# Optimization experiments

Measured on AMD Instinct MI355X. Metric: run time of the kernel, lower is better.

## Reference

```python
import jax, jax.numpy as jnp
import numpy as np

V, E, HD, NT = 50001, 256, 512, 24   # vocab, embed_dim, hidden_dim, tag_size
H = HD // 2                          # per-direction LSTM hidden
B, S = 64, 512


def setup_inputs() -> dict:
    key = jax.random.key(0)
    ks = jax.random.split(key, 18)
    lw = lambda k, sh, s=0.05: (jax.random.normal(k, sh, jnp.float32) * s)
    x = jax.random.randint(ks[0], (B, S), 0, V).astype(jnp.int32)
    lengths = jax.random.randint(ks[1], (B,), S // 2, S + 1)
    mask = jnp.arange(S)[None, :] < lengths[:, None]  # [B,S] bool, mask[:,0]=True
    return {
        "x": x,
        "mask": mask,
        "emb": lw(ks[2], (V, E), 0.1),
        "Wih_f": lw(ks[3], (4 * H, E)), "Whh_f": lw(ks[4], (4 * H, H)),
        "bih_f": lw(ks[5], (4 * H,)), "bhh_f": lw(ks[6], (4 * H,)),
        "Wih_b": lw(ks[7], (4 * H, E)), "Whh_b": lw(ks[8], (4 * H, H)),
        "bih_b": lw(ks[9], (4 * H,)), "bhh_b": lw(ks[10], (4 * H,)),
        "Wout": lw(ks[11], (NT, HD)), "bout": lw(ks[12], (NT,)),
        "trans": lw(ks[13], (NT, NT), 0.1),
        "start": lw(ks[14], (NT,), 0.1),
        "end": lw(ks[15], (NT,), 0.1),
    }


def _lstm_dir(xs, Wih, Whh, bih, bhh):
    # xs: [S, B, E] -> hs: [S, B, H]; torch gate order i, f, g, o
    Bn = xs.shape[1]
    h0 = jnp.zeros((Bn, H), xs.dtype)

    def step(carry, xt):
        h, c = carry
        g = xt @ Wih.T + h @ Whh.T + bih + bhh
        i, f, gg, o = jnp.split(g, 4, axis=-1)
        c = jax.nn.sigmoid(f) * c + jax.nn.sigmoid(i) * jnp.tanh(gg)
        h = jax.nn.sigmoid(o) * jnp.tanh(c)
        return (h, c), h

    _, hs = jax.lax.scan(step, (h0, h0), xs)
    return hs


def _viterbi(emissions, mask, trans, start, end):
    # emissions: [B, S, T]; mask: [B, S] bool. Returns (tags [B,S] int, best_score [B]).
    em = emissions.transpose(1, 0, 2)   # [S, B, T]
    mk = mask.transpose(1, 0)           # [S, B]
    nT = trans.shape[0]
    idx_id = jnp.arange(nT)[None, :]    # identity backpointers for padded steps
    score = start[None, :] + em[0]      # [B, T]

    def step(score, inp):
        e_t, m_t = inp
        cand = score[:, :, None] + trans[None, :, :] + e_t[:, None, :]  # [B,Tprev,Tnext]
        idx = jnp.argmax(cand, axis=1)
        best = jnp.max(cand, axis=1)
        idx = jnp.where(m_t[:, None], idx, idx_id)
        new_score = jnp.where(m_t[:, None], best, score)
        return new_score, idx

    score, hist = jax.lax.scan(step, score, (em[1:], mk[1:]))  # hist: [S-1, B, T]
    final = score + end[None, :]
    last_tag = jnp.argmax(final, axis=1)   # [B]
    best_score = jnp.max(final, axis=1)    # [B]

    def back(tag, h_t):
        prev = jnp.take_along_axis(h_t, tag[:, None], axis=1)[:, 0]
        return prev, tag

    tag0, ys = jax.lax.scan(back, last_tag, hist, reverse=True)
    tags = jnp.concatenate([tag0[None, :], ys], axis=0).T  # [B, S]
    return tags, best_score


def reference(x, mask, emb, Wih_f, Whh_f, bih_f, bhh_f, Wih_b, Whh_b, bih_b, bhh_b,
              Wout, bout, trans, start, end):
    e = emb[x]                      # [B, S, E] embedding gather
    xs = e.transpose(1, 0, 2)       # [S, B, E] time-major for scan
    hf = _lstm_dir(xs, Wih_f, Whh_f, bih_f, bhh_f)
    hb = jnp.flip(_lstm_dir(jnp.flip(xs, 0), Wih_b, Whh_b, bih_b, bhh_b), 0)
    h = jnp.concatenate([hf, hb], axis=-1)          # [S, B, HD]
    emis = (h @ Wout.T + bout).transpose(1, 0, 2)   # [B, S, T]
    tags, _ = _viterbi(emis, mask, trans, start, end)
    return tags
```

## Files before the change

### kernel.cpp

```cpp
#include <hip/hip_runtime.h>
#include <math.h>

#define B_   64
#define S_   512
#define E_   256
#define H_   256
#define G4H_ 1024
#define NT_  24

static const size_t HBUF_OFF  = 0;
static const size_t CST_OFF   = 131072;
static const size_t EMF_OFF   = 163840;
static const size_t EMB_OFF   = 950272;
static const size_t HOUT_OFF  = 1736704;

__device__ __forceinline__ float sigmoidf_(float x) {
  return 1.0f / (1.0f + expf(-x));
}

__global__ __launch_bounds__(256) void k1_xpre(
    const int* __restrict__ x, const float* __restrict__ emb,
    const float* __restrict__ Wih_f, const float* __restrict__ bih_f,
    const float* __restrict__ bhh_f, const float* __restrict__ Wih_b,
    const float* __restrict__ bih_b, const float* __restrict__ bhh_b,
    float* __restrict__ xpre_c, int chunk, int tc)
{
  __shared__ float As[32][132];
  __shared__ float Bs[32][132];
  __shared__ int   xt[128];

  const int tid = threadIdx.x;
  const int wg  = blockIdx.x;
  const int per_dir = 4 * tc;
  const int d   = wg / per_dir;
  const int rem = wg % per_dir;
  const int m0  = (rem >> 3) * 128;
  const int n0  = (rem & 7) * 128;
  const int t0  = chunk * tc;

  const float* Wih = d ? Wih_b : Wih_f;
  const float* bih = d ? bih_b : bih_f;
  const float* bhh = d ? bhh_b : bhh_f;

  if (tid < 128) {
    int m = m0 + tid;
    int lt = m >> 6, b = m & 63;
    int tok = d ? (S_ - 1 - (t0 + lt)) : (t0 + lt);
    xt[tid] = x[b * S_ + tok];
  }
  __syncthreads();

  float acc[8][8];
#pragma unroll
  for (int i = 0; i < 8; ++i)
#pragma unroll
    for (int j = 0; j < 8; ++j) acc[i][j] = 0.0f;

  const int mt8 = tid & 15;
  const int nt8 = tid >> 4;
  const int q = tid & 7, rbase = tid >> 3;

  for (int kc = 0; kc < 8; ++kc) {
    const int k0 = kc * 32;
#pragma unroll
    for (int i = 0; i < 4; ++i) {
      int row = rbase + i * 32;
      float4 a = *(const float4*)(emb + (long)xt[row] * E_ + k0 + q * 4);
      As[q * 4 + 0][row] = a.x; As[q * 4 + 1][row] = a.y;
      As[q * 4 + 2][row] = a.z; As[q * 4 + 3][row] = a.w;
      float4 w = *(const float4*)(Wih + (long)(n0 + row) * E_ + k0 + q * 4);
      Bs[q * 4 + 0][row] = w.x; Bs[q * 4 + 1][row] = w.y;
      Bs[q * 4 + 2][row] = w.z; Bs[q * 4 + 3][row] = w.w;
    }
    __syncthreads();
#pragma unroll
    for (int k = 0; k < 32; ++k) {
      float4 a0 = *(float4*)&As[k][mt8 * 8];
      float4 a1 = *(float4*)&As[k][mt8 * 8 + 4];
      float4 b0 = *(float4*)&Bs[k][nt8 * 8];
      float4 b1 = *(float4*)&Bs[k][nt8 * 8 + 4];
      float am[8] = {a0.x, a0.y, a0.z, a0.w, a1.x, a1.y, a1.z, a1.w};
      float bn[8] = {b0.x, b0.y, b0.z, b0.w, b1.x, b1.y, b1.z, b1.w};
#pragma unroll
      for (int i = 0; i < 8; ++i)
#pragma unroll
        for (int j = 0; j < 8; ++j) acc[i][j] = fmaf(am[i], bn[j], acc[i][j]);
    }
    __syncthreads();
  }

  float bias[8];
  {
    float4 u0 = *(const float4*)(bih + n0 + nt8 * 8);
    float4 u1 = *(const float4*)(bih + n0 + nt8 * 8 + 4);
    float4 v0 = *(const float4*)(bhh + n0 + nt8 * 8);
    float4 v1 = *(const float4*)(bhh + n0 + nt8 * 8 + 4);
    bias[0] = u0.x + v0.x; bias[1] = u0.y + v0.y; bias[2] = u0.z + v0.z;
    bias[3] = u0.w + v0.w; bias[4] = u1.x + v1.x; bias[5] = u1.y + v1.y;
    bias[6] = u1.z + v1.z; bias[7] = u1.w + v1.w;
  }
#pragma unroll
  for (int i = 0; i < 8; ++i) {
    int m = m0 + mt8 * 8 + i;
    int lt = m >> 6, b = m & 63;
    float* o = xpre_c + ((size_t)(d * tc + lt) * B_ + b) * G4H_ + n0 + nt8 * 8;
    float4 r0, r1;
    r0.x = acc[i][0] + bias[0]; r0.y = acc[i][1] + bias[1];
    r0.z = acc[i][2] + bias[2]; r0.w = acc[i][3] + bias[3];
    r1.x = acc[i][4] + bias[4]; r1.y = acc[i][5] + bias[5];
    r1.z = acc[i][6] + bias[6]; r1.w = acc[i][7] + bias[7];
    *(float4*)o = r0;
    *(float4*)(o + 4) = r1;
  }
}

__global__ __launch_bounds__(256, 1) void k2_lstm(
    const float* __restrict__ Whh_f, const float* __restrict__ Whh_b,
    const float* __restrict__ xpre_c, float* __restrict__ hout_c,
    unsigned long long* hbuf, float* cstate, int chunk, int tc)
{
  __shared__ float hTb[16][260];
  __shared__ float part[2][4][16][36];

  const int tid = threadIdx.x;
  const int wg  = blockIdx.x;
  const int d   = wg >> 7;
  const int bg  = (wg >> 5) & 3;
  const int s   = wg & 31;
  const int b0  = bg * 16;
  const float* Whh = d ? Whh_b : Whh_f;

  const int w     = tid >> 6;
  const int lane  = tid & 63;
  const int bl16  = lane & 15;
  const int kb    = lane >> 4;
  const int kbase = w * 64 + kb * 16;
  const int ks    = tid >> 5;
  const int tl    = tid & 31, bt = tl & 3, rt = tl >> 2;
  const int pbl   = tid >> 3, pj = tid & 7;

  float wreg[4][32];
#pragma unroll
  for (int ri = 0; ri < 4; ++ri) {
    int r = rt * 4 + ri, g = r >> 3, j = r & 7;
    const float* src = Whh + ((size_t)(g * H_ + s * 8 + j)) * H_ + ks * 32;
#pragma unroll
    for (int q = 0; q < 8; ++q) {
      float4 v = *(const float4*)(src + q * 4);
      wreg[ri][q * 4 + 0] = v.x; wreg[ri][q * 4 + 1] = v.y;
      wreg[ri][q * 4 + 2] = v.z; wreg[ri][q * 4 + 3] = v.w;
    }
  }

  float c_reg = 0.0f;
  if (chunk > 0 && tid < 128)
    c_reg = cstate[((size_t)d * B_ + b0 + pbl) * H_ + s * 8 + pj];

  for (int tt = 1; tt <= tc; ++tt) {
    const int t  = chunk * tc + tt;
    const int lt = tt - 1;
    const int p  = tt & 1;

    float xp[4];
    if (tid < 128) {
#pragma unroll
      for (int g = 0; g < 4; ++g)
        xp[g] = xpre_c[((size_t)(d * tc + lt) * B_ + b0 + pbl) * G4H_ +
                       g * H_ + s * 8 + pj];
    }

    {
      const unsigned expt = (unsigned)(t - 1);
      const unsigned long long* hb =
          hbuf + ((size_t)(((t - 1) & 1) * 2 + d)) * (256 * 64);
      const size_t a0 = (size_t)kbase * 64 + b0 + bl16;
      unsigned long long e[16];
#pragma unroll
      for (int i = 0; i < 16; ++i)
        e[i] = __hip_atomic_load(hb + a0 + (size_t)i * 64,
                                 __ATOMIC_RELAXED, __HIP_MEMORY_SCOPE_AGENT);
      int lim = 0;
      while (true) {
        unsigned bad = 0;
#pragma unroll
        for (int i = 0; i < 16; ++i)
          if ((unsigned)(e[i] >> 32) != expt) bad |= (1u << i);
        if (bad == 0) break;
        if (++lim > (1 << 18)) break;
#pragma unroll
        for (int i = 0; i < 16; ++i)
          if (bad & (1u << i))
            e[i] = __hip_atomic_load(hb + a0 + (size_t)i * 64,
                                     __ATOMIC_RELAXED,
                                     __HIP_MEMORY_SCOPE_AGENT);
      }
      float4 v0, v1, v2, v3;
      v0.x = __uint_as_float((unsigned)e[0]);  v0.y = __uint_as_float((unsigned)e[1]);
      v0.z = __uint_as_float((unsigned)e[2]);  v0.w = __uint_as_float((unsigned)e[3]);
      v1.x = __uint_as_float((unsigned)e[4]);  v1.y = __uint_as_float((unsigned)e[5]);
      v1.z = __uint_as_float((unsigned)e[6]);  v1.w = __uint_as_float((unsigned)e[7]);
      v2.x = __uint_as_float((unsigned)e[8]);  v2.y = __uint_as_float((unsigned)e[9]);
      v2.z = __uint_as_float((unsigned)e[10]); v2.w = __uint_as_float((unsigned)e[11]);
      v3.x = __uint_as_float((unsigned)e[12]); v3.y = __uint_as_float((unsigned)e[13]);
      v3.z = __uint_as_float((unsigned)e[14]); v3.w = __uint_as_float((unsigned)e[15]);
      *(float4*)&hTb[bl16][kbase +  0] = v0;
      *(float4*)&hTb[bl16][kbase +  4] = v1;
      *(float4*)&hTb[bl16][kbase +  8] = v2;
      *(float4*)&hTb[bl16][kbase + 12] = v3;
    }

    float acc[4][4];
#pragma unroll
    for (int bi = 0; bi < 4; ++bi)
#pragma unroll
      for (int ri = 0; ri < 4; ++ri) acc[bi][ri] = 0.0f;
#pragma unroll
    for (int kq = 0; kq < 8; ++kq) {
      const int k0 = ks * 32 + kq * 4;
      float4 h4[4];
#pragma unroll
      for (int bi = 0; bi < 4; ++bi)
        h4[bi] = *(float4*)&hTb[bt * 4 + bi][k0];
#pragma unroll
      for (int kk = 0; kk < 4; ++kk) {
#pragma unroll
        for (int bi = 0; bi < 4; ++bi) {
          const float hv = kk == 0 ? h4[bi].x : kk == 1 ? h4[bi].y
                         : kk == 2 ? h4[bi].z : h4[bi].w;
#pragma unroll
          for (int ri = 0; ri < 4; ++ri)
            acc[bi][ri] = fmaf(hv, wreg[ri][kq * 4 + kk], acc[bi][ri]);
        }
      }
    }
#pragma unroll
    for (int bi = 0; bi < 4; ++bi)
#pragma unroll
      for (int ri = 0; ri < 4; ++ri)
        acc[bi][ri] += __shfl_xor(acc[bi][ri], 32, 64);
    if (lane < 32) {
#pragma unroll
      for (int bi = 0; bi < 4; ++bi) {
        float4 v = make_float4(acc[bi][0], acc[bi][1], acc[bi][2], acc[bi][3]);
        *(float4*)&part[p][w][bt * 4 + bi][rt * 4] = v;
      }
    }
    __syncthreads();

    if (tid < 128) {
      const int bglob = b0 + pbl;
      float gsum[4];
#pragma unroll
      for (int g = 0; g < 4; ++g) {
        const int r = g * 8 + pj;
        gsum[g] = xp[g] + ((part[p][0][pbl][r] + part[p][1][pbl][r]) +
                           (part[p][2][pbl][r] + part[p][3][pbl][r]));
      }
      float si = sigmoidf_(gsum[0]);
      float sf = sigmoidf_(gsum[1]);
      float tg = tanhf(gsum[2]);
      float so = sigmoidf_(gsum[3]);
      c_reg = sf * c_reg + si * tg;
      float h = so * tanhf(c_reg);
      unsigned long long pk =
          (((unsigned long long)(unsigned)t) << 32) |
          (unsigned long long)__float_as_uint(h);
      __hip_atomic_store(hbuf + ((size_t)((t & 1) * 2 + d)) * (256 * 64) +
                             (size_t)(s * 8 + pj) * 64 + bglob,
                         pk, __ATOMIC_RELAXED, __HIP_MEMORY_SCOPE_AGENT);
      hout_c[((size_t)(d * tc + lt) * B_ + bglob) * H_ + s * 8 + pj] = h;
    }
  }

  if (tid < 128)
    cstate[((size_t)d * B_ + b0 + pbl) * H_ + s * 8 + pj] = c_reg;
}

__global__ __launch_bounds__(256) void k3_emis(
    const float* __restrict__ hout_c, const float* __restrict__ Wout,
    float* __restrict__ emisF, float* __restrict__ emisB, int chunk, int tc)
{
  __shared__ float hh[8][264];
  const int tid = threadIdx.x;
  const int nt8 = tc >> 3;
  const int per_d = 64 * nt8;
  const int d   = blockIdx.x / per_d;
  const int rem = blockIdx.x % per_d;
  const int b   = rem / nt8;
  const int lt0 = (rem % nt8) * 8;
  float* emisX = d ? emisB : emisF;
  {
    int r = tid >> 5, q = tid & 31;
    const float* src = hout_c + ((size_t)(d * tc + lt0 + r) * B_ + b) * H_;
#pragma unroll
    for (int i = 0; i < 2; ++i) {
      int f4i = q + 32 * i;
      *(float4*)&hh[r][f4i * 4] = *(const float4*)(src + f4i * 4);
    }
  }
  __syncthreads();
  if (tid < 192) {
    int r = tid / 24, tag = tid % 24;
    float acc = 0.0f;
    const float* w = Wout + (size_t)tag * 512 + d * 256;
#pragma unroll 4
    for (int k4 = 0; k4 < 64; ++k4) {
      float4 wv = *(const float4*)(w + k4 * 4);
      float4 hv = *(const float4*)&hh[r][k4 * 4];
      acc = fmaf(wv.x, hv.x, acc);
      acc = fmaf(wv.y, hv.y, acc);
      acc = fmaf(wv.z, hv.z, acc);
      acc = fmaf(wv.w, hv.w, acc);
    }
    int lt = lt0 + r;
    int tok = d ? (S_ - 1 - (chunk * tc + lt)) : (chunk * tc + lt);
    emisX[((size_t)b * S_ + tok) * NT_ + tag] = acc;
  }
}

__global__ __launch_bounds__(64) void k4_viterbi(
    const float* __restrict__ emisF, const float* __restrict__ emisB,
    const float* __restrict__ bout, const unsigned char* __restrict__ mb,
    const float* __restrict__ trans, const float* __restrict__ startv,
    const float* __restrict__ endv, int* __restrict__ outp)
{
  __shared__ float tl[24 * 25];
  __shared__ float sc[24];
  __shared__ float fin[24];
  __shared__ unsigned char hist[511 * 24];
  const int b = blockIdx.x;
  const int tid = threadIdx.x;
  const int is_bool = mb[1];

  for (int i = tid; i < 576; i += 64) tl[(i / 24) * 25 + (i % 24)] = trans[i];
  if (tid < 24) {
    size_t e0 = (size_t)b * S_ * NT_ + tid;
    sc[tid] = startv[tid] + (emisF[e0] + emisB[e0] + bout[tid]);
  }
  __syncthreads();

  for (int t = 1; t < S_; ++t) {
    float best = -3.4e38f, scj = 0.f;
    int idx = 0;
    int m;
    {
      int mi = b * S_ + t;
      m = is_bool ? (int)mb[mi] : (int)mb[mi << 2];
    }
    if (tid < 24) {
      size_t ei = ((size_t)b * S_ + t) * NT_ + tid;
      float e = emisF[ei] + emisB[ei] + bout[tid];
      for (int i = 0; i < 24; ++i) {
        float v = (sc[i] + tl[i * 25 + tid]) + e;
        if (v > best) { best = v; idx = i; }
      }
      scj = sc[tid];
    }
    __syncthreads();
    if (tid < 24) {
      sc[tid] = m ? best : scj;
      hist[(t - 1) * 24 + tid] = (unsigned char)(m ? idx : tid);
    }
    __syncthreads();
  }
  if (tid < 24) fin[tid] = sc[tid] + endv[tid];
  __syncthreads();
  if (tid == 0) {
    int tag = 0; float best = fin[0];
    for (int i = 1; i < 24; ++i)
      if (fin[i] > best) { best = fin[i]; tag = i; }
    outp[b * S_ + (S_ - 1)] = tag;
    for (int tt = S_ - 2; tt >= 0; --tt) {
      tag = hist[tt * 24 + tag];
      outp[b * S_ + tt] = tag;
    }
  }
}

extern "C" void kernel_launch(void* const* d_in, const int* in_sizes, int n_in,
                              void* d_out, int out_size, void* d_ws,
                              size_t ws_size, hipStream_t stream)
{
  const int*   x      = (const int*)d_in[0];
  const unsigned char* maskb = (const unsigned char*)d_in[1];
  const float* emb    = (const float*)d_in[2];
  const float* Wih_f  = (const float*)d_in[3];
  const float* Whh_f  = (const float*)d_in[4];
  const float* bih_f  = (const float*)d_in[5];
  const float* bhh_f  = (const float*)d_in[6];
  const float* Wih_b  = (const float*)d_in[7];
  const float* Whh_b  = (const float*)d_in[8];
  const float* bih_b  = (const float*)d_in[9];
  const float* bhh_b  = (const float*)d_in[10];
  const float* Wout   = (const float*)d_in[11];
  const float* bout   = (const float*)d_in[12];
  const float* trans  = (const float*)d_in[13];
  const float* startv = (const float*)d_in[14];
  const float* endv   = (const float*)d_in[15];

  int tc = 8;
  {
    const int cand[6] = {512, 256, 128, 64, 32, 16};
    for (int i = 0; i < 6; ++i) {
      size_t needF = HOUT_OFF + (size_t)cand[i] * (2 * B_ * H_ + 2 * B_ * G4H_);
      if (needF * sizeof(float) <= ws_size) { tc = cand[i]; break; }
    }
  }
  const int nc = S_ / tc;

  float* ws     = (float*)d_ws;
  unsigned long long* hbuf = (unsigned long long*)(ws + HBUF_OFF);
  float* cstate = ws + CST_OFF;
  float* emisF  = ws + EMF_OFF;
  float* emisB  = ws + EMB_OFF;
  float* hout_c = ws + HOUT_OFF;
  float* xpre_c = hout_c + (size_t)tc * 2 * B_ * H_;

  hipMemsetAsync(d_ws, 0, 131072 * sizeof(float), stream);

  for (int c = 0; c < nc; ++c) {
    hipLaunchKernelGGL(k1_xpre, dim3(8 * tc), dim3(256), 0, stream,
                       x, emb, Wih_f, bih_f, bhh_f, Wih_b, bih_b, bhh_b,
                       xpre_c, c, tc);
    hipLaunchKernelGGL(k2_lstm, dim3(256), dim3(256), 0, stream,
                       Whh_f, Whh_b, xpre_c, hout_c, hbuf, cstate, c, tc);
    hipLaunchKernelGGL(k3_emis, dim3(2 * 64 * (tc / 8)), dim3(256), 0, stream,
                       hout_c, Wout, emisF, emisB, c, tc);
  }
  hipLaunchKernelGGL(k4_viterbi, dim3(64), dim3(64), 0, stream,
                     emisF, emisB, bout, maskb, trans, startv, endv,
                     (int*)d_out);
}
```

Baseline: 2.885 ms.

## Give each wave its own batch slice in LSTM step to drop block barrier

Restructures the recurrent LSTM kernel so each of the four waves owns 4 batch rows and the full K=256 reduction, instead of splitting K across waves. Partial sums are reduced with intra-wave shuffles, and the per-step __syncthreads plus the cross-wave shared-memory reduction are removed. A rotated k order in the weight load and h reads is added to reduce LDS bank conflicts. The trade-off is three shuffle rounds per accumulator in place of one, and reliance on wave-synchronous LDS visibility between the gbuf write and read within a wave.

```diff
diff --git a/kernel.cpp b/kernel.cpp
--- a/kernel.cpp
+++ b/kernel.cpp
@@ -119,53 +119,50 @@
     const float* __restrict__ xpre_c, float* __restrict__ hout_c,
     unsigned long long* hbuf, float* cstate, int chunk, int tc)
 {
-  __shared__ float hTb[16][260];
-  __shared__ float part[2][4][16][36];
-
-  const int tid = threadIdx.x;
-  const int wg  = blockIdx.x;
-  const int d   = wg >> 7;
-  const int bg  = (wg >> 5) & 3;
-  const int s   = wg & 31;
-  const int b0  = bg * 16;
+  __shared__ float hTb[4][4][264];
+  __shared__ float gbuf[4][4][36];
+
+  const int tid  = threadIdx.x;
+  const int wg   = blockIdx.x;
+  const int d    = wg >> 7;
+  const int bg   = (wg >> 5) & 3;
+  const int s    = wg & 31;
   const float* Whh = d ? Whh_b : Whh_f;
 
-  const int w     = tid >> 6;
-  const int lane  = tid & 63;
-  const int bl16  = lane & 15;
-  const int kb    = lane >> 4;
-  const int kbase = w * 64 + kb * 16;
-  const int ks    = tid >> 5;
-  const int tl    = tid & 31, bt = tl & 3, rt = tl >> 2;
-  const int pbl   = tid >> 3, pj = tid & 7;
+  const int w    = tid >> 6;
+  const int lane = tid & 63;
+  const int bw   = bg * 16 + 4 * w;
+  const int kg = lane >> 3, rp = lane & 7;
+  const int sb = lane & 3, ksec = lane >> 2;
+  const int pb = (lane >> 3) & 3, pj = lane & 7;
 
   float wreg[4][32];
 #pragma unroll
   for (int ri = 0; ri < 4; ++ri) {
-    int r = rt * 4 + ri, g = r >> 3, j = r & 7;
-    const float* src = Whh + ((size_t)(g * H_ + s * 8 + j)) * H_ + ks * 32;
+    int r = rp * 4 + ri, g = r >> 3, j = r & 7;
+    const float* src = Whh + ((size_t)(g * H_ + s * 8 + j)) * H_ + kg * 32;
 #pragma unroll
     for (int q = 0; q < 8; ++q) {
-      float4 v = *(const float4*)(src + q * 4);
+      int qs = (q + kg * 2) & 7;
+      float4 v = *(const float4*)(src + qs * 4);
       wreg[ri][q * 4 + 0] = v.x; wreg[ri][q * 4 + 1] = v.y;
       wreg[ri][q * 4 + 2] = v.z; wreg[ri][q * 4 + 3] = v.w;
     }
   }
 
   float c_reg = 0.0f;
-  if (chunk > 0 && tid < 128)
-    c_reg = cstate[((size_t)d * B_ + b0 + pbl) * H_ + s * 8 + pj];
+  if (chunk > 0 && lane < 32)
+    c_reg = cstate[((size_t)d * B_ + bw + pb) * H_ + s * 8 + pj];
 
   for (int tt = 1; tt <= tc; ++tt) {
     const int t  = chunk * tc + tt;
     const int lt = tt - 1;
-    const int p  = tt & 1;
 
     float xp[4];
-    if (tid < 128) {
+    if (lane < 32) {
 #pragma unroll
       for (int g = 0; g < 4; ++g)
-        xp[g] = xpre_c[((size_t)(d * tc + lt) * B_ + b0 + pbl) * G4H_ +
+        xp[g] = xpre_c[((size_t)(d * tc + lt) * B_ + bw + pb) * G4H_ +
                        g * H_ + s * 8 + pj];
     }
 
@@ -173,7 +170,7 @@
       const unsigned expt = (unsigned)(t - 1);
       const unsigned long long* hb =
           hbuf + ((size_t)(((t - 1) & 1) * 2 + d)) * (256 * 64);
-      const size_t a0 = (size_t)kbase * 64 + b0 + bl16;
+      const size_t a0 = (size_t)(ksec * 16) * 64 + (bw + sb);
       unsigned long long e[16];
 #pragma unroll
       for (int i = 0; i < 16; ++i)
@@ -194,68 +191,62 @@
                                      __ATOMIC_RELAXED,
                                      __HIP_MEMORY_SCOPE_AGENT);
       }
-      float4 v0, v1, v2, v3;
-      v0.x = __uint_as_float((unsigned)e[0]);  v0.y = __uint_as_float((unsigned)e[1]);
-      v0.z = __uint_as_float((unsigned)e[2]);  v0.w = __uint_as_float((unsigned)e[3]);
-      v1.x = __uint_as_float((unsigned)e[4]);  v1.y = __uint_as_float((unsigned)e[5]);
-      v1.z = __uint_as_float((unsigned)e[6]);  v1.w = __uint_as_float((unsigned)e[7]);
-      v2.x = __uint_as_float((unsigned)e[8]);  v2.y = __uint_as_float((unsigned)e[9]);
-      v2.z = __uint_as_float((unsigned)e[10]); v2.w = __uint_as_float((unsigned)e[11]);
-      v3.x = __uint_as_float((unsigned)e[12]); v3.y = __uint_as_float((unsigned)e[13]);
-      v3.z = __uint_as_float((unsigned)e[14]); v3.w = __uint_as_float((unsigned)e[15]);
-      *(float4*)&hTb[bl16][kbase +  0] = v0;
-      *(float4*)&hTb[bl16][kbase +  4] = v1;
-      *(float4*)&hTb[bl16][kbase +  8] = v2;
-      *(float4*)&hTb[bl16][kbase + 12] = v3;
+#pragma unroll
+      for (int n = 0; n < 4; ++n) {
+        float4 v;
+        v.x = __uint_as_float((unsigned)e[4 * n + 0]);
+        v.y = __uint_as_float((unsigned)e[4 * n + 1]);
+        v.z = __uint_as_float((unsigned)e[4 * n + 2]);
+        v.w = __uint_as_float((unsigned)e[4 * n + 3]);
+        *(float4*)&hTb[w][sb][ksec * 16 + n * 4] = v;
+      }
     }
 
     float acc[4][4];
 #pragma unroll
-    for (int bi = 0; bi < 4; ++bi)
-#pragma unroll
-      for (int ri = 0; ri < 4; ++ri) acc[bi][ri] = 0.0f;
-#pragma unroll
-    for (int kq = 0; kq < 8; ++kq) {
-      const int k0 = ks * 32 + kq * 4;
-      float4 h4[4];
-#pragma unroll
-      for (int bi = 0; bi < 4; ++bi)
-        h4[bi] = *(float4*)&hTb[bt * 4 + bi][k0];
-#pragma unroll
-      for (int kk = 0; kk < 4; ++kk) {
-#pragma unroll
-        for (int bi = 0; bi < 4; ++bi) {
-          const float hv = kk == 0 ? h4[bi].x : kk == 1 ? h4[bi].y
-                         : kk == 2 ? h4[bi].z : h4[bi].w;
+    for (int b = 0; b < 4; ++b)
+#pragma unroll
+      for (int ri = 0; ri < 4; ++ri) acc[b][ri] = 0.0f;
+#pragma unroll
+    for (int b = 0; b < 4; ++b) {
+      const float* hrow = &hTb[w][b][kg * 32];
+#pragma unroll
+      for (int q = 0; q < 8; ++q) {
+        int qs = (q + kg * 2) & 7;
+        float4 h4 = *(const float4*)(hrow + qs * 4);
+#pragma unroll
+        for (int kk = 0; kk < 4; ++kk) {
+          const float hv = kk == 0 ? h4.x : kk == 1 ? h4.y
+                         : kk == 2 ? h4.z : h4.w;
 #pragma unroll
           for (int ri = 0; ri < 4; ++ri)
-            acc[bi][ri] = fmaf(hv, wreg[ri][kq * 4 + kk], acc[bi][ri]);
+            acc[b][ri] = fmaf(hv, wreg[ri][q * 4 + kk], acc[b][ri]);
         }
       }
     }
 #pragma unroll
-    for (int bi = 0; bi < 4; ++bi)
-#pragma unroll
-      for (int ri = 0; ri < 4; ++ri)
-        acc[bi][ri] += __shfl_xor(acc[bi][ri], 32, 64);
+    for (int b = 0; b < 4; ++b)
+#pragma unroll
+      for (int ri = 0; ri < 4; ++ri) {
+        float v = acc[b][ri];
+        v += __shfl_xor(v, 8, 64);
+        v += __shfl_xor(v, 16, 64);
+        v += __shfl_xor(v, 32, 64);
+        acc[b][ri] = v;
+      }
+    if (kg == 0) {
+#pragma unroll
+      for (int b = 0; b < 4; ++b)
+        *(float4*)&gbuf[w][b][rp * 4] =
+            make_float4(acc[b][0], acc[b][1], acc[b][2], acc[b][3]);
+    }
+
     if (lane < 32) {
-#pragma unroll
-      for (int bi = 0; bi < 4; ++bi) {
-        float4 v = make_float4(acc[bi][0], acc[bi][1], acc[bi][2], acc[bi][3]);
-        *(float4*)&part[p][w][bt * 4 + bi][rt * 4] = v;
-      }
-    }
-    __syncthreads();
-
-    if (tid < 128) {
-      const int bglob = b0 + pbl;
+      const int bglob = bw + pb;
       float gsum[4];
 #pragma unroll
-      for (int g = 0; g < 4; ++g) {
-        const int r = g * 8 + pj;
-        gsum[g] = xp[g] + ((part[p][0][pbl][r] + part[p][1][pbl][r]) +
-                           (part[p][2][pbl][r] + part[p][3][pbl][r]));
-      }
+      for (int g = 0; g < 4; ++g)
+        gsum[g] = xp[g] + gbuf[w][pb][g * 8 + pj];
       float si = sigmoidf_(gsum[0]);
       float sf = sigmoidf_(gsum[1]);
       float tg = tanhf(gsum[2]);
@@ -272,8 +263,8 @@
     }
   }
 
-  if (tid < 128)
-    cstate[((size_t)d * B_ + b0 + pbl) * H_ + s * 8 + pj] = c_reg;
+  if (lane < 32)
+    cstate[((size_t)d * B_ + bw + pb) * H_ + s * 8 + pj] = c_reg;
 }
 
 __global__ __launch_bounds__(256) void k3_emis(
```

New measurement: 4.461 ms. 1.55x slower.

## Use split-bf16 MFMA for input projection GEMM

Applied to the files above, without the earlier changes.

Replaces the FP32 FMA tiled GEMM that computes the input-gate preactivations with a bf16 MFMA version. Both operands are split into hi and lo bf16 parts, and three or four MFMAs per tile recover near-FP32 accuracy. A new pre-kernel converts Wih into the hi/lo bf16 arrays once per call. Workspace offsets shift to make room for these arrays. The sequential LSTM kernel likely dominates runtime, so the overall effect is limited. The output stores are scalar and strided rather than vectorized.

```diff
diff --git a/kernel.cpp b/kernel.cpp
--- a/kernel.cpp
+++ b/kernel.cpp
@@ -10,24 +10,58 @@
 
 static const size_t HBUF_OFF  = 0;
 static const size_t CST_OFF   = 131072;
-static const size_t EMF_OFF   = 163840;
-static const size_t EMB_OFF   = 950272;
-static const size_t HOUT_OFF  = 1736704;
+static const size_t WHI_OFF   = 163840;
+static const size_t WLO_OFF   = 425984;
+static const size_t EMF_OFF   = 688128;
+static const size_t EMB_OFF   = 1474560;
+static const size_t HOUT_OFF  = 2260992;
+
+typedef short  bf16x8_ __attribute__((ext_vector_type(8)));
+typedef float  f32x4_  __attribute__((ext_vector_type(4)));
 
 __device__ __forceinline__ float sigmoidf_(float x) {
   return 1.0f / (1.0f + expf(-x));
 }
 
-__global__ __launch_bounds__(256) void k1_xpre(
+__device__ __forceinline__ unsigned short bf16_rne_(float v) {
+  unsigned u = __float_as_uint(v);
+  unsigned r = u + 0x7fffu + ((u >> 16) & 1u);
+  return (unsigned short)(r >> 16);
+}
+
+__global__ __launch_bounds__(256) void k0_wconv(
+    const float* __restrict__ Wf, const float* __restrict__ Wb,
+    unsigned short* __restrict__ whi, unsigned short* __restrict__ wlo)
+{
+  int idx = blockIdx.x * 256 + threadIdx.x;
+  int d   = idx >> 16;
+  int i4  = idx & 65535;
+  const float* W = d ? Wb : Wf;
+  float4 v = *(const float4*)(W + (size_t)i4 * 4);
+  float vv[4] = {v.x, v.y, v.z, v.w};
+  unsigned short h[4], l[4];
+#pragma unroll
+  for (int e = 0; e < 4; ++e) {
+    h[e] = bf16_rne_(vv[e]);
+    float hf = __uint_as_float((unsigned)h[e] << 16);
+    l[e] = bf16_rne_(vv[e] - hf);
+  }
+  size_t o = (size_t)d * 262144 + (size_t)i4 * 4;
+  whi[o + 0] = h[0]; whi[o + 1] = h[1]; whi[o + 2] = h[2]; whi[o + 3] = h[3];
+  wlo[o + 0] = l[0]; wlo[o + 1] = l[1]; wlo[o + 2] = l[2]; wlo[o + 3] = l[3];
+}
+
+__global__ __launch_bounds__(256) void k1_xpre_mfma(
     const int* __restrict__ x, const float* __restrict__ emb,
-    const float* __restrict__ Wih_f, const float* __restrict__ bih_f,
-    const float* __restrict__ bhh_f, const float* __restrict__ Wih_b,
+    const unsigned short* __restrict__ whi,
+    const unsigned short* __restrict__ wlo,
+    const float* __restrict__ bih_f, const float* __restrict__ bhh_f,
     const float* __restrict__ bih_b, const float* __restrict__ bhh_b,
     float* __restrict__ xpre_c, int chunk, int tc)
 {
-  __shared__ float As[32][132];
-  __shared__ float Bs[32][132];
-  __shared__ int   xt[128];
+  __shared__ unsigned short Ahi[128][40], Alo[128][40];
+  __shared__ unsigned short Bhi[128][40], Blo[128][40];
+  __shared__ int xt[128];
 
   const int tid = threadIdx.x;
   const int wg  = blockIdx.x;
@@ -38,9 +72,10 @@
   const int n0  = (rem & 7) * 128;
   const int t0  = chunk * tc;
 
-  const float* Wih = d ? Wih_b : Wih_f;
   const float* bih = d ? bih_b : bih_f;
   const float* bhh = d ? bhh_b : bhh_f;
+  const unsigned short* Whi = whi + (size_t)d * 262144;
+  const unsigned short* Wlo = wlo + (size_t)d * 262144;
 
   if (tid < 128) {
     int m = m0 + tid;
@@ -48,70 +83,95 @@
     int tok = d ? (S_ - 1 - (t0 + lt)) : (t0 + lt);
     xt[tid] = x[b * S_ + tok];
   }
-  __syncthreads();
-
-  float acc[8][8];
-#pragma unroll
-  for (int i = 0; i < 8; ++i)
-#pragma unroll
-    for (int j = 0; j < 8; ++j) acc[i][j] = 0.0f;
-
-  const int mt8 = tid & 15;
-  const int nt8 = tid >> 4;
-  const int q = tid & 7, rbase = tid >> 3;
-
-  for (int kc = 0; kc < 8; ++kc) {
-    const int k0 = kc * 32;
-#pragma unroll
-    for (int i = 0; i < 4; ++i) {
-      int row = rbase + i * 32;
-      float4 a = *(const float4*)(emb + (long)xt[row] * E_ + k0 + q * 4);
-      As[q * 4 + 0][row] = a.x; As[q * 4 + 1][row] = a.y;
-      As[q * 4 + 2][row] = a.z; As[q * 4 + 3][row] = a.w;
-      float4 w = *(const float4*)(Wih + (long)(n0 + row) * E_ + k0 + q * 4);
-      Bs[q * 4 + 0][row] = w.x; Bs[q * 4 + 1][row] = w.y;
-      Bs[q * 4 + 2][row] = w.z; Bs[q * 4 + 3][row] = w.w;
-    }
+
+  const int lane = tid & 63, wid = tid >> 6;
+  const int wr = wid >> 1, wc = wid & 1;
+  const int fr = lane & 15, fq = lane >> 4;
+  const int sr = tid >> 1, sh = tid & 1;
+
+  f32x4_ acc[4][4];
+#pragma unroll
+  for (int i = 0; i < 4; ++i)
+#pragma unroll
+    for (int j = 0; j < 4; ++j) acc[i][j] = (f32x4_){0.f, 0.f, 0.f, 0.f};
+
+  for (int slab = 0; slab < 8; ++slab) {
+    const int k0 = slab * 32;
     __syncthreads();
-#pragma unroll
-    for (int k = 0; k < 32; ++k) {
-      float4 a0 = *(float4*)&As[k][mt8 * 8];
-      float4 a1 = *(float4*)&As[k][mt8 * 8 + 4];
-      float4 b0 = *(float4*)&Bs[k][nt8 * 8];
-      float4 b1 = *(float4*)&Bs[k][nt8 * 8 + 4];
-      float am[8] = {a0.x, a0.y, a0.z, a0.w, a1.x, a1.y, a1.z, a1.w};
-      float bn[8] = {b0.x, b0.y, b0.z, b0.w, b1.x, b1.y, b1.z, b1.w};
-#pragma unroll
-      for (int i = 0; i < 8; ++i)
-#pragma unroll
-        for (int j = 0; j < 8; ++j) acc[i][j] = fmaf(am[i], bn[j], acc[i][j]);
+    {
+      const float* src = emb + (size_t)xt[sr] * E_ + k0 + sh * 16;
+      unsigned short h[16], l[16];
+#pragma unroll
+      for (int q = 0; q < 4; ++q) {
+        float4 v = *(const float4*)(src + q * 4);
+        float vv[4] = {v.x, v.y, v.z, v.w};
+#pragma unroll
+        for (int e = 0; e < 4; ++e) {
+          h[q * 4 + e] = bf16_rne_(vv[e]);
+          float hf = __uint_as_float((unsigned)h[q * 4 + e] << 16);
+          l[q * 4 + e] = bf16_rne_(vv[e] - hf);
+        }
+      }
+      *(bf16x8_*)&Ahi[sr][sh * 16 + 0] = *(bf16x8_*)&h[0];
+      *(bf16x8_*)&Ahi[sr][sh * 16 + 8] = *(bf16x8_*)&h[8];
+      *(bf16x8_*)&Alo[sr][sh * 16 + 0] = *(bf16x8_*)&l[0];
+      *(bf16x8_*)&Alo[sr][sh * 16 + 8] = *(bf16x8_*)&l[8];
+    }
+    {
+      const size_t o = (size_t)(n0 + sr) * E_ + k0 + sh * 16;
+      *(bf16x8_*)&Bhi[sr][sh * 16 + 0] = *(const bf16x8_*)(Whi + o);
+      *(bf16x8_*)&Bhi[sr][sh * 16 + 8] = *(const bf16x8_*)(Whi + o + 8);
+      *(bf16x8_*)&Blo[sr][sh * 16 + 0] = *(const bf16x8_*)(Wlo + o);
+      *(bf16x8_*)&Blo[sr][sh * 16 + 8] = *(const bf16x8_*)(Wlo + o + 8);
     }
     __syncthreads();
-  }
-
-  float bias[8];
-  {
-    float4 u0 = *(const float4*)(bih + n0 + nt8 * 8);
-    float4 u1 = *(const float4*)(bih + n0 + nt8 * 8 + 4);
-    float4 v0 = *(const float4*)(bhh + n0 + nt8 * 8);
-    float4 v1 = *(const float4*)(bhh + n0 + nt8 * 8 + 4);
-    bias[0] = u0.x + v0.x; bias[1] = u0.y + v0.y; bias[2] = u0.z + v0.z;
-    bias[3] = u0.w + v0.w; bias[4] = u1.x + v1.x; bias[5] = u1.y + v1.y;
-    bias[6] = u1.z + v1.z; bias[7] = u1.w + v1.w;
-  }
-#pragma unroll
-  for (int i = 0; i < 8; ++i) {
-    int m = m0 + mt8 * 8 + i;
-    int lt = m >> 6, b = m & 63;
-    float* o = xpre_c + ((size_t)(d * tc + lt) * B_ + b) * G4H_ + n0 + nt8 * 8;
-    float4 r0, r1;
-    r0.x = acc[i][0] + bias[0]; r0.y = acc[i][1] + bias[1];
-    r0.z = acc[i][2] + bias[2]; r0.w = acc[i][3] + bias[3];
-    r1.x = acc[i][4] + bias[4]; r1.y = acc[i][5] + bias[5];
-    r1.z = acc[i][6] + bias[6]; r1.w = acc[i][7] + bias[7];
-    *(float4*)o = r0;
-    *(float4*)(o + 4) = r1;
-  }
+
+    bf16x8_ ah[4], al[4], bh[4], bl[4];
+#pragma unroll
+    for (int mi = 0; mi < 4; ++mi) {
+      int row = 64 * wr + mi * 16 + fr;
+      ah[mi] = *(bf16x8_*)&Ahi[row][fq * 8];
+      al[mi] = *(bf16x8_*)&Alo[row][fq * 8];
+    }
+#pragma unroll
+    for (int ni = 0; ni < 4; ++ni) {
+      int row = 64 * wc + ni * 16 + fr;
+      bh[ni] = *(bf16x8_*)&Bhi[row][fq * 8];
+      bl[ni] = *(bf16x8_*)&Blo[row][fq * 8];
+    }
+#pragma unroll
+    for (int mi = 0; mi < 4; ++mi)
+#pragma unroll
+      for (int ni = 0; ni < 4; ++ni) {
+        acc[mi][ni] = __builtin_amdgcn_mfma_f32_16x16x32_bf16(
+            al[mi], bl[ni], acc[mi][ni], 0, 0, 0);
+        acc[mi][ni] = __builtin_amdgcn_mfma_f32_16x16x32_bf16(
+            al[mi], bh[ni], acc[mi][ni], 0, 0, 0);
+        acc[mi][ni] = __builtin_amdgcn_mfma_f32_16x16x32_bf16(
+            ah[mi], bl[ni], acc[mi][ni], 0, 0, 0);
+        acc[mi][ni] = __builtin_amdgcn_mfma_f32_16x16x32_bf16(
+            ah[mi], bh[ni], acc[mi][ni], 0, 0, 0);
+      }
+  }
+
+  float bias[4];
+#pragma unroll
+  for (int ni = 0; ni < 4; ++ni) {
+    int col = n0 + 64 * wc + ni * 16 + fr;
+    bias[ni] = bih[col] + bhh[col];
+  }
+  const size_t base = (size_t)(d * tc * 64) * G4H_;
+#pragma unroll
+  for (int mi = 0; mi < 4; ++mi)
+#pragma unroll
+    for (int ni = 0; ni < 4; ++ni) {
+      int col = n0 + 64 * wc + ni * 16 + fr;
+#pragma unroll
+      for (int r = 0; r < 4; ++r) {
+        int m = m0 + 64 * wr + mi * 16 + fq * 4 + r;
+        xpre_c[base + (size_t)m * G4H_ + col] = acc[mi][ni][r] + bias[ni];
+      }
+    }
 }
 
 __global__ __launch_bounds__(256, 1) void k2_lstm(
@@ -411,16 +471,20 @@
   float* ws     = (float*)d_ws;
   unsigned long long* hbuf = (unsigned long long*)(ws + HBUF_OFF);
   float* cstate = ws + CST_OFF;
+  unsigned short* whi = (unsigned short*)(ws + WHI_OFF);
+  unsigned short* wlo = (unsigned short*)(ws + WLO_OFF);
   float* emisF  = ws + EMF_OFF;
   float* emisB  = ws + EMB_OFF;
   float* hout_c = ws + HOUT_OFF;
   float* xpre_c = hout_c + (size_t)tc * 2 * B_ * H_;
 
   hipMemsetAsync(d_ws, 0, 131072 * sizeof(float), stream);
+  hipLaunchKernelGGL(k0_wconv, dim3(512), dim3(256), 0, stream,
+                     Wih_f, Wih_b, whi, wlo);
 
   for (int c = 0; c < nc; ++c) {
-    hipLaunchKernelGGL(k1_xpre, dim3(8 * tc), dim3(256), 0, stream,
-                       x, emb, Wih_f, bih_f, bhh_f, Wih_b, bih_b, bhh_b,
+    hipLaunchKernelGGL(k1_xpre_mfma, dim3(8 * tc), dim3(256), 0, stream,
+                       x, emb, whi, wlo, bih_f, bhh_f, bih_b, bhh_b,
                        xpre_c, c, tc);
     hipLaunchKernelGGL(k2_lstm, dim3(256), dim3(256), 0, stream,
                        Whh_f, Whh_b, xpre_c, hout_c, hbuf, cstate, c, tc);
```

Result: faster. 2.670 ms (-7.4%).
